# Kernel optimization log

Measured on AMD Instinct MI355X. Metric: run time of the kernel, lower is better.

Reference implementation:

```python
import jax, jax.numpy as jnp
import numpy as np
from jax import lax

FH, FW, STRIDE = 100, 160, 16
IMG_H, IMG_W = FH * STRIDE, FW * STRIDE
A = 9
PRE_NMS, POST_NMS = 6000, 300  # prediction-path caps (training=0)
IOU_THR = 0.7
NEG = jnp.float32(-1e9)


def _make_anchor_map():
    # classic 3 scales x 3 aspect ratios, stride-16 grid, (y1,x1,y2,x2)
    scales = np.array([128.0, 256.0, 512.0], np.float32)
    ratios = np.array([0.5, 1.0, 2.0], np.float32)
    hs = (scales[:, None] * np.sqrt(ratios)[None, :]).reshape(-1)  # [9]
    ws = (scales[:, None] / np.sqrt(ratios)[None, :]).reshape(-1)
    cy = ((np.arange(FH, dtype=np.float32) + 0.5) * STRIDE)[:, None, None]
    cx = ((np.arange(FW, dtype=np.float32) + 0.5) * STRIDE)[None, :, None]
    y1 = np.broadcast_to(cy - 0.5 * hs, (FH, FW, A))
    x1 = np.broadcast_to(cx - 0.5 * ws, (FH, FW, A))
    y2 = np.broadcast_to(cy + 0.5 * hs, (FH, FW, A))
    x2 = np.broadcast_to(cx + 0.5 * ws, (FH, FW, A))
    am = np.stack([y1, x1, y2, x2], axis=-1)  # [FH,FW,9,4]
    return jnp.asarray(am.reshape(1, FH, FW, A * 4))


def setup_inputs() -> dict:
    key = jax.random.key(0)
    ks = jax.random.split(key, 6)
    return {
        "input_image": jax.random.uniform(ks[0], (1, IMG_H, IMG_W, 3), jnp.float32),
        "feature_map": jax.random.normal(ks[1], (1, FH, FW, 512), jnp.float32),
        "anchor_map": _make_anchor_map(),
        "anchor_valid_map": jnp.ones((1, FH, FW, A), jnp.float32),
        "W1": 0.01 * jax.random.normal(ks[2], (3, 3, 512, 512), jnp.float32),
        "b1": jnp.zeros((512,), jnp.float32),
        "Wc": 0.01 * jax.random.normal(ks[3], (1, 1, 512, A), jnp.float32),
        "bc": jnp.zeros((A,), jnp.float32),
        "Wr": 0.01 * jax.random.normal(ks[4], (1, 1, 512, 4 * A), jnp.float32),
        "br": jnp.zeros((4 * A,), jnp.float32),
        "training": 0,
    }


def _conv(x, w, b):
    return lax.conv_general_dilated(
        x, w, (1, 1), "SAME", dimension_numbers=("NHWC", "HWIO", "NHWC")
    ) + b


def _iou_one_vs_all(box, boxes):
    yy1 = jnp.maximum(box[0], boxes[:, 0])
    xx1 = jnp.maximum(box[1], boxes[:, 1])
    yy2 = jnp.minimum(box[2], boxes[:, 2])
    xx2 = jnp.minimum(box[3], boxes[:, 3])
    inter = jnp.maximum(yy2 - yy1, 0.0) * jnp.maximum(xx2 - xx1, 0.0)
    a1 = jnp.maximum(box[2] - box[0], 0.0) * jnp.maximum(box[3] - box[1], 0.0)
    a2 = jnp.maximum(boxes[:, 2] - boxes[:, 0], 0.0) * jnp.maximum(boxes[:, 3] - boxes[:, 1], 0.0)
    return inter / (a1 + a2 - inter + 1e-8)


def _nms(boxes, scores, max_out, iou_thr):
    # greedy NMS with fixed iteration count (padded with zero boxes)
    def step(s, _):
        i = jnp.argmax(s)
        best = s[i]
        box = boxes[i]
        valid = best > NEG * 0.5
        ious = _iou_one_vs_all(box, boxes)
        s = jnp.where(ious > iou_thr, NEG, s)
        s = s.at[i].set(NEG)
        out = jnp.where(valid, box, jnp.zeros_like(box))
        return s, out

    _, sel = lax.scan(step, scores, None, length=max_out)
    return sel  # [max_out, 4]


def reference(input_image, feature_map, anchor_map, anchor_valid_map,
              W1, b1, Wc, bc, Wr, br, training):
    pre_nms = 12000 if training else PRE_NMS
    post_nms = 2000 if training else POST_NMS
    # RPN head convs
    y = jax.nn.relu(_conv(feature_map, W1, b1))
    scores_map = jax.nn.sigmoid(_conv(y, Wc, bc))          # [1,FH,FW,9]
    reg_map = _conv(y, Wr, br)                              # [1,FH,FW,36]
    # flatten (extract_valid)
    anchors = anchor_map.reshape(-1, 4)                     # [N,4] (y1,x1,y2,x2)
    obj = scores_map.reshape(-1)                            # [N]
    deltas = reg_map.reshape(-1, 4)                         # [N,4] (ty,tx,th,tw)
    # delta -> bbox decode (means=0, stds=1)
    ah = anchors[:, 2] - anchors[:, 0]
    aw = anchors[:, 3] - anchors[:, 1]
    acy = anchors[:, 0] + 0.5 * ah
    acx = anchors[:, 1] + 0.5 * aw
    cy = acy + deltas[:, 0] * ah
    cx = acx + deltas[:, 1] * aw
    h = ah * jnp.exp(deltas[:, 2])
    w = aw * jnp.exp(deltas[:, 3])
    props = jnp.stack([cy - 0.5 * h, cx - 0.5 * w, cy + 0.5 * h, cx + 0.5 * w], axis=1)
    # sort desc by score, keep top pre_nms
    sc, idx = lax.top_k(obj, pre_nms)
    props = props[idx]
    # clip to image
    img_h = jnp.float32(input_image.shape[1])
    img_w = jnp.float32(input_image.shape[2])
    tl = jnp.maximum(props[:, 0:2], 0.0)
    y2 = jnp.minimum(props[:, 2], img_h)[:, None]
    x2 = jnp.minimum(props[:, 3], img_w)[:, None]
    props = jnp.concatenate([tl, y2, x2], axis=1)
    # min-size filter (>=16 on each side), via score masking (jit-safe)
    hh = props[:, 2] - props[:, 0]
    ww = props[:, 3] - props[:, 1]
    sc = jnp.where((hh >= 16.0) & (ww >= 16.0), sc, NEG)
    proposals = _nms(props, sc, post_nms, IOU_THR)          # [post_nms,4], zero-padded
    return scores_map, reg_map, proposals
```

## Files before the change

### kernel.cpp

```cpp
#include <hip/hip_runtime.h>
#include <math.h>

#define FHh 100
#define FWw 160
#define CIN 512
#define COUT 512
#define NPIX 16000
#define NANCH 144000
#define PRE_NMS 6000
#define POST_NMS 300
#define EQCAP 8192

typedef double d4 __attribute__((ext_vector_type(4)));

__device__ __forceinline__ unsigned fkey(float x){
  unsigned b = __float_as_uint(x);
  return (b & 0x80000000u) ? ~b : (b | 0x80000000u);
}
__device__ __forceinline__ unsigned long long dkey(double x){
  unsigned long long u = (unsigned long long)__double_as_longlong(x);
  return (u & 0x8000000000000000ull) ? ~u : (u | 0x8000000000000000ull);
}
__device__ __forceinline__ unsigned long long shfl_u64(unsigned long long x, int lane){
  unsigned lo = (unsigned)x, hi = (unsigned)(x >> 32);
  lo = __shfl(lo, lane, 64);
  hi = __shfl(hi, lane, 64);
  return ((unsigned long long)hi << 32) | lo;
}
__device__ __forceinline__ void gload_lds16(const void* g, void* l){
  __builtin_amdgcn_global_load_lds(
      (const __attribute__((address_space(1))) void*)g,
      (__attribute__((address_space(3))) void*)l, 16, 0, 0);
}

__global__ __launch_bounds__(256) void prep_all(
    const float* __restrict__ Wc, const float* __restrict__ Wr, const float* __restrict__ W1,
    double* __restrict__ WcT, double* __restrict__ WrT, double* __restrict__ W64)
{
  const int bid = blockIdx.x;
  if (bid < 90){
    const int gid = bid*256 + threadIdx.x;
    const int n = gid >> 9, ci = gid & 511;
    if (n < 9) WcT[(size_t)n*512 + ci] = (double)Wc[ci*9 + n];
    else       WrT[(size_t)(n-9)*512 + ci] = (double)Wr[ci*36 + (n-9)];
  } else {
    const int i = (bid - 90)*256 + threadIdx.x;
    const float4 v = ((const float4*)W1)[i];
    double2* d = (double2*)(W64 + (size_t)i*4);
    d[0] = make_double2((double)v.x, (double)v.y);
    d[1] = make_double2((double)v.z, (double)v.w);
  }
}

__global__ __launch_bounds__(256, 2) void conv_gemm(
    const float* __restrict__ fm, const double* __restrict__ W64,
    const float* __restrict__ b1, double* __restrict__ yd)
{
  __shared__ double Ns[16*204];
  __shared__ double Bsh[2][16*128];

  const int bid  = blockIdx.x;
  const int cg   = bid / 125;
  const int tile = bid - cg*125;
  const int rp   = tile / 5;
  const int xseg = tile - rp*5;
  const int x0   = xseg*32;
  const int row0 = rp*4;
  const int co0  = cg*128;

  const int tid  = threadIdx.x;
  const int lane = tid & 63;
  const int kl   = lane >> 4;
  const int cl   = lane & 15;
  const int wv   = tid >> 6;
  const int wr   = wv >> 1;
  const int wc   = wv & 1;

  double pf[4][4];

  auto APF_LOAD = [&](int kc){
    #pragma unroll
    for (int it = 0; it < 4; ++it){
      const int t  = it*256 + tid;
      const int px = t >> 2, kq = t & 3;
      const int nr = px / 34, nc = px - nr*34;
      const int row = row0 + nr - 1, col = x0 + nc - 1;
      const bool ok = (t < 816) && (row >= 0) && (row < FHh) && (col >= 0) && (col < FWw);
      if (ok){
        const float4 v = *(const float4*)(fm + ((size_t)(row*FWw + col))*CIN + kc*16 + kq*4);
        pf[it][0] = (double)v.x; pf[it][1] = (double)v.y;
        pf[it][2] = (double)v.z; pf[it][3] = (double)v.w;
      } else {
        pf[it][0] = pf[it][1] = pf[it][2] = pf[it][3] = 0.0;
      }
    }
  };
  auto APF_WRITE = [&](){
    #pragma unroll
    for (int it = 0; it < 4; ++it){
      const int t  = it*256 + tid;
      const int px = t >> 2, kq = t & 3;
      if (t < 816){
        #pragma unroll
        for (int u = 0; u < 4; ++u)
          Ns[(kq*4 + u)*204 + px] = pf[it][u];
      }
    }
  };
  auto BGLDS = [&](int buf, int tap, int kc){
    #pragma unroll
    for (int s = 0; s < 4; ++s){
      const int g    = s*256 + tid;
      const int krow = g >> 6;
      const int co2  = (g & 63)*2;
      const double* src = W64 + ((size_t)(tap*512 + kc*16 + krow))*512 + co0 + co2;
      gload_lds16(src, &Bsh[buf][krow*128 + co2]);
    }
  };

  d4 acc[4][4];
  #pragma unroll
  for (int mt = 0; mt < 4; ++mt)
    #pragma unroll
    for (int nt = 0; nt < 4; ++nt) acc[mt][nt] = (d4){0.0, 0.0, 0.0, 0.0};

  APF_LOAD(0);
  BGLDS(0, 0, 0);
  APF_WRITE();
  __syncthreads();

  const int abase_t = kl*204 + cl;
  const int bbase_t = kl*128 + wc*64 + cl;

  for (int kc = 0; kc < 32; ++kc){
    #pragma unroll 1
    for (int tap = 0; tap < 9; ++tap){
      const int ph  = kc*9 + tap;
      const int cur = ph & 1;
      if (ph + 1 < 288){
        const int ntap = (tap == 8) ? 0 : tap + 1;
        const int nkc  = (tap == 8) ? kc + 1 : kc;
        BGLDS(cur ^ 1, ntap, nkc);
      }
      if (tap == 7 && kc < 31) APF_LOAD(kc + 1);
      const int ty = tap / 3;
      const int dy = ty - 1, dx = (tap - ty*3) - 1;
      const double* An = Ns + abase_t + (wr*2 + dy + 1)*34 + (dx + 1);
      const double* Bn = Bsh[cur] + bbase_t;
      #pragma unroll
      for (int k4 = 0; k4 < 4; ++k4){
        const double a0 = An[k4*4*204 + 0*34 + 0];
        const double a1 = An[k4*4*204 + 0*34 + 16];
        const double a2 = An[k4*4*204 + 1*34 + 0];
        const double a3 = An[k4*4*204 + 1*34 + 16];
        const double b0 = Bn[k4*4*128 + 0];
        const double b1v= Bn[k4*4*128 + 16];
        const double b2 = Bn[k4*4*128 + 32];
        const double b3 = Bn[k4*4*128 + 48];
        acc[0][0] = __builtin_amdgcn_mfma_f64_16x16x4f64(a0, b0,  acc[0][0], 0, 0, 0);
        acc[0][1] = __builtin_amdgcn_mfma_f64_16x16x4f64(a0, b1v, acc[0][1], 0, 0, 0);
        acc[0][2] = __builtin_amdgcn_mfma_f64_16x16x4f64(a0, b2,  acc[0][2], 0, 0, 0);
        acc[0][3] = __builtin_amdgcn_mfma_f64_16x16x4f64(a0, b3,  acc[0][3], 0, 0, 0);
        acc[1][0] = __builtin_amdgcn_mfma_f64_16x16x4f64(a1, b0,  acc[1][0], 0, 0, 0);
        acc[1][1] = __builtin_amdgcn_mfma_f64_16x16x4f64(a1, b1v, acc[1][1], 0, 0, 0);
        acc[1][2] = __builtin_amdgcn_mfma_f64_16x16x4f64(a1, b2,  acc[1][2], 0, 0, 0);
        acc[1][3] = __builtin_amdgcn_mfma_f64_16x16x4f64(a1, b3,  acc[1][3], 0, 0, 0);
        acc[2][0] = __builtin_amdgcn_mfma_f64_16x16x4f64(a2, b0,  acc[2][0], 0, 0, 0);
        acc[2][1] = __builtin_amdgcn_mfma_f64_16x16x4f64(a2, b1v, acc[2][1], 0, 0, 0);
        acc[2][2] = __builtin_amdgcn_mfma_f64_16x16x4f64(a2, b2,  acc[2][2], 0, 0, 0);
        acc[2][3] = __builtin_amdgcn_mfma_f64_16x16x4f64(a2, b3,  acc[2][3], 0, 0, 0);
        acc[3][0] = __builtin_amdgcn_mfma_f64_16x16x4f64(a3, b0,  acc[3][0], 0, 0, 0);
        acc[3][1] = __builtin_amdgcn_mfma_f64_16x16x4f64(a3, b1v, acc[3][1], 0, 0, 0);
        acc[3][2] = __builtin_amdgcn_mfma_f64_16x16x4f64(a3, b2,  acc[3][2], 0, 0, 0);
        acc[3][3] = __builtin_amdgcn_mfma_f64_16x16x4f64(a3, b3,  acc[3][3], 0, 0, 0);
      }
      __syncthreads();
      if (tap == 8 && kc < 31){
        APF_WRITE();
        __syncthreads();
      }
    }
  }
  double bb[4];
  #pragma unroll
  for (int nt = 0; nt < 4; ++nt) bb[nt] = (double)b1[co0 + wc*64 + nt*16 + cl];
  #pragma unroll
  for (int mt = 0; mt < 4; ++mt){
    #pragma unroll
    for (int i = 0; i < 4; ++i){
      const int pxl = wr*64 + mt*16 + 4*i + kl;
      const int gpx = (row0 + (pxl >> 5))*FWw + x0 + (pxl & 31);
      double* yrow = yd + (size_t)gpx*CIN + co0 + wc*64 + cl;
      #pragma unroll
      for (int nt = 0; nt < 4; ++nt){
        yrow[nt*16] = fmax(acc[mt][nt][i] + bb[nt], 0.0);
      }
    }
  }
}

__global__ __launch_bounds__(256) void head2(
    const double* __restrict__ yd, const double* __restrict__ WcT, const float* __restrict__ bc,
    const double* __restrict__ WrT, const float* __restrict__ br,
    float* __restrict__ out, double* __restrict__ scored, double* __restrict__ regd)
{
  __shared__ double yl[8192];
  const int bid = blockIdx.x, t = threadIdx.x;
  const double2* src = (const double2*)(yd + (size_t)bid * 8192);
  double2* dst = (double2*)yl;
  for (int j = t; j < 4096; j += 256) dst[j] = src[j];
  __syncthreads();
  if (t < 180){
    const int n  = t % 45;
    const int pq = t / 45;
    const double* w = (n < 9) ? (WcT + (size_t)n*512) : (WrT + (size_t)(n-9)*512);
    const double* y0 = yl + (pq*4+0)*512;
    const double* y1 = yl + (pq*4+1)*512;
    const double* y2 = yl + (pq*4+2)*512;
    const double* y3 = yl + (pq*4+3)*512;
    double s0=0.0, s1=0.0, s2=0.0, s3=0.0;
    for (int ci = 0; ci < 512; ++ci){
      const double wv = w[ci];
      s0 = fma(y0[ci], wv, s0);
      s1 = fma(y1[ci], wv, s1);
      s2 = fma(y2[ci], wv, s2);
      s3 = fma(y3[ci], wv, s3);
    }
    const double sv[4] = {s0, s1, s2, s3};
    if (n < 9){
      const double bb = (double)bc[n];
      #pragma unroll
      for (int u = 0; u < 4; ++u){
        const double s = sv[u] + bb;
        const double sig = 1.0 / (1.0 + exp(-s));
        const int gi = (bid*16 + pq*4 + u)*9 + n;
        out[gi] = (float)sig;
        scored[gi] = sig;
      }
    } else {
      const int m = n - 9;
      const double bb = (double)br[m];
      #pragma unroll
      for (int u = 0; u < 4; ++u){
        const double s = sv[u] + bb;
        const int gi = (bid*16 + pq*4 + u)*36 + m;
        out[144000 + gi] = (float)s;
        regd[gi] = s;
      }
    }
  }
}

__global__ __launch_bounds__(256) void decode_hist(
    const float* __restrict__ amap, const double* __restrict__ scored,
    const double* __restrict__ regd, double* __restrict__ boxesd,
    unsigned* __restrict__ key32, unsigned long long* __restrict__ nmskey,
    unsigned* __restrict__ hist)
{
  const int i = blockIdx.x*256 + threadIdx.x;
  if (i >= NANCH) return;
  const double a0=(double)amap[4*i+0], a1=(double)amap[4*i+1];
  const double a2=(double)amap[4*i+2], a3=(double)amap[4*i+3];
  const double d0=regd[4*i+0], d1=regd[4*i+1], d2=regd[4*i+2], d3=regd[4*i+3];
  const double ah = a2 - a0, aw = a3 - a1;
  const double cy = a0 + 0.5*ah + d0*ah;
  const double cx = a1 + 0.5*aw + d1*aw;
  const double h = ah * exp(d2), w = aw * exp(d3);
  double y1 = cy - 0.5*h, x1 = cx - 0.5*w, y2 = cy + 0.5*h, x2 = cx + 0.5*w;
  y1 = fmax(y1, 0.0); x1 = fmax(x1, 0.0);
  y2 = fmin(y2, 1600.0); x2 = fmin(x2, 2560.0);
  boxesd[4*i+0]=y1; boxesd[4*i+1]=x1; boxesd[4*i+2]=y2; boxesd[4*i+3]=x2;
  const double obj = scored[i];
  const bool ok = (y2 - y1 >= 16.0) && (x2 - x1 >= 16.0);
  const unsigned k32 = fkey((float)obj);
  key32[i] = k32;
  nmskey[i] = ok ? dkey(obj) : dkey(-1e9);
  atomicAdd(&hist[k32 >> 16], 1u);
}

__global__ __launch_bounds__(1024) void scan_hi(const unsigned* __restrict__ hist, int* __restrict__ meta){
  __shared__ unsigned part[1024];
  const int t = threadIdx.x;
  unsigned s = 0;
  for (int j = 0; j < 64; ++j) s += hist[65535 - (t*64 + j)];
  part[t] = s;
  __syncthreads();
  for (int off = 1; off < 1024; off <<= 1){
    unsigned v = (t >= off) ? part[t - off] : 0u;
    __syncthreads();
    part[t] += v;
    __syncthreads();
  }
  const unsigned incl = part[t], excl = incl - s;
  if (excl < PRE_NMS && incl >= PRE_NMS){
    unsigned cum = excl;
    for (int j = 0; j < 64; ++j){
      const int bin = 65535 - (t*64 + j);
      const unsigned c = hist[bin];
      if (cum + c >= PRE_NMS){ meta[0] = bin; meta[1] = (int)cum; break; }
      cum += c;
    }
  }
}

__global__ __launch_bounds__(256) void hist_lo(const unsigned* __restrict__ key,
                                               const int* __restrict__ meta, unsigned* __restrict__ hist){
  const int i = blockIdx.x*256 + threadIdx.x;
  if (i < NANCH){
    const unsigned k = key[i];
    if ((int)(k >> 16) == meta[0]) atomicAdd(&hist[k & 0xFFFFu], 1u);
  }
}

__global__ __launch_bounds__(1024) void scan_lo(const unsigned* __restrict__ hist, int* __restrict__ meta){
  __shared__ unsigned part[1024];
  const int t = threadIdx.x;
  const unsigned G0 = (unsigned)meta[1];
  unsigned s = 0;
  for (int j = 0; j < 64; ++j) s += hist[65535 - (t*64 + j)];
  part[t] = s;
  __syncthreads();
  for (int off = 1; off < 1024; off <<= 1){
    unsigned v = (t >= off) ? part[t - off] : 0u;
    __syncthreads();
    part[t] += v;
    __syncthreads();
  }
  const unsigned incl = G0 + part[t], excl = incl - s;
  if (excl < PRE_NMS && incl >= PRE_NMS){
    unsigned cum = excl;
    for (int j = 0; j < 64; ++j){
      const int bin = 65535 - (t*64 + j);
      const unsigned c = hist[bin];
      if (cum + c >= PRE_NMS){
        meta[2] = (int)(((unsigned)meta[0] << 16) | (unsigned)bin);
        meta[3] = (int)cum;
        meta[4] = PRE_NMS - (int)cum;
        break;
      }
      cum += c;
    }
  }
}

__global__ __launch_bounds__(256) void compact_k(
    const unsigned* __restrict__ key, const unsigned long long* __restrict__ nmskey,
    const double* __restrict__ boxesd, const int* __restrict__ meta,
    int* __restrict__ cnt, double* __restrict__ selboxd,
    unsigned long long* __restrict__ selkey, int* __restrict__ eqidx)
{
  const int i = blockIdx.x*256 + threadIdx.x;
  if (i >= NANCH) return;
  const unsigned k = key[i];
  const unsigned T = (unsigned)meta[2];
  if (k > T){
    const int s = atomicAdd(&cnt[0], 1);
    selboxd[4*s+0]=boxesd[4*i+0]; selboxd[4*s+1]=boxesd[4*i+1];
    selboxd[4*s+2]=boxesd[4*i+2]; selboxd[4*s+3]=boxesd[4*i+3];
    selkey[s] = nmskey[i];
  } else if (k == T){
    const int e = atomicAdd(&cnt[1], 1);
    if (e < EQCAP) eqidx[e] = i;
  }
}

__global__ __launch_bounds__(256) void rankeq(
    const double* __restrict__ scored, const double* __restrict__ boxesd,
    const unsigned long long* __restrict__ nmskey,
    const int* __restrict__ meta, const int* __restrict__ cnt,
    const int* __restrict__ eqidx, double* __restrict__ selboxd,
    unsigned long long* __restrict__ selkey)
{
  __shared__ int eq[EQCAP];
  const int t = threadIdx.x;
  int E = cnt[1]; if (E > EQCAP) E = EQCAP;
  const int R = meta[4], G2 = meta[3];
  for (int j = t; j < E; j += 256) eq[j] = eqidx[j];
  __syncthreads();
  for (int j = t; j < E; j += 256){
    const int my = eq[j];
    const double smy = scored[my];
    int rank = 0;
    for (int k2 = 0; k2 < E; ++k2){
      const int ok = eq[k2];
      const double sk = scored[ok];
      rank += ((sk > smy) || (sk == smy && ok < my)) ? 1 : 0;
    }
    if (rank < R){
      const int s = G2 + rank;
      selboxd[4*s+0]=boxesd[4*my+0]; selboxd[4*s+1]=boxesd[4*my+1];
      selboxd[4*s+2]=boxesd[4*my+2]; selboxd[4*s+3]=boxesd[4*my+3];
      selkey[s] = nmskey[my];
    }
  }
}

__global__ __launch_bounds__(256) void rank_scatter(
    const unsigned long long* __restrict__ selkey, const double* __restrict__ selboxd,
    unsigned long long* __restrict__ skeys, double* __restrict__ sboxd)
{
  __shared__ unsigned long long k[PRE_NMS];
  const int t = threadIdx.x;
  for (int j = t; j < PRE_NMS; j += 256) k[j] = selkey[j];
  __syncthreads();
  const int j = blockIdx.x*256 + t;
  if (j >= PRE_NMS) return;
  const unsigned long long kj = k[j];
  int r = 0;
  for (int i = 0; i < PRE_NMS; i += 4){
    r += (int)((k[i+0] > kj) || (k[i+0] == kj && (i+0) < j));
    r += (int)((k[i+1] > kj) || (k[i+1] == kj && (i+1) < j));
    r += (int)((k[i+2] > kj) || (k[i+2] == kj && (i+2) < j));
    r += (int)((k[i+3] > kj) || (k[i+3] == kj && (i+3) < j));
  }
  skeys[r] = kj;
  sboxd[(size_t)r*4+0] = selboxd[(size_t)j*4+0];
  sboxd[(size_t)r*4+1] = selboxd[(size_t)j*4+1];
  sboxd[(size_t)r*4+2] = selboxd[(size_t)j*4+2];
  sboxd[(size_t)r*4+3] = selboxd[(size_t)j*4+3];
}

__global__ __launch_bounds__(256) void iou_bitmap(
    const double* __restrict__ sboxd, unsigned long long* __restrict__ rowbits)
{
  __shared__ double cbx[4096];
  const int g = blockIdx.y;
  const int r0 = blockIdx.x * 16;
  const int t = threadIdx.x;
  const int cbase = g * 1024;
  for (int e = t; e < 4096; e += 256){
    const int bi = cbase + (e >> 2);
    cbx[e] = (bi < PRE_NMS) ? sboxd[(size_t)bi*4 + (e & 3)] : 0.0;
  }
  __syncthreads();
  const int r = r0 + (t >> 4);
  const int w = t & 15;
  const double by1 = sboxd[(size_t)r*4+0], bx1 = sboxd[(size_t)r*4+1];
  const double by2 = sboxd[(size_t)r*4+2], bx2 = sboxd[(size_t)r*4+3];
  const double a1 = fmax(by2-by1, 0.0) * fmax(bx2-bx1, 0.0);
  unsigned long long bits = 0ull;
  for (int b = 0; b < 64; ++b){
    const int bcol = (b + w) & 63;
    const int j = cbase + w*64 + bcol;
    if (j < PRE_NMS){
      const int ce = (w*64 + bcol)*4;
      const double c0 = cbx[ce+0], c1 = cbx[ce+1], c2 = cbx[ce+2], c3 = cbx[ce+3];
      const double yy1 = fmax(by1, c0), xx1 = fmax(bx1, c1);
      const double yy2 = fmin(by2, c2), xx2 = fmin(bx2, c3);
      const double inter = fmax(yy2-yy1, 0.0) * fmax(xx2-xx1, 0.0);
      const double a2 = fmax(c2-c0, 0.0) * fmax(c3-c1, 0.0);
      const double iou = inter / (a1 + a2 - inter + 1e-8);
      if (iou > 0.7) bits |= (1ull << bcol);
    }
  }
  rowbits[(size_t)r*128 + g*16 + w] = bits;
}

__global__ __launch_bounds__(64) void greedy(
    const unsigned long long* __restrict__ skeys, const double* __restrict__ sboxd,
    const unsigned long long* __restrict__ rowbits, float* __restrict__ outp)
{
  const int t = threadIdx.x;
  const unsigned long long KEYTH = dkey(-5.0e8);
  int bad = PRE_NMS;
  for (int j = t; j < PRE_NMS; j += 64){
    if (skeys[j] <= KEYTH){ bad = j; break; }
  }
  #pragma unroll
  for (int off = 32; off > 0; off >>= 1){
    const int o = __shfl_down(bad, off, 64);
    bad = (o < bad) ? o : bad;
  }
  const int ilim = __builtin_amdgcn_readfirstlane(bad);

  unsigned long long s0 = 0ull, s1 = 0ull;
  int emitted = 0;
  for (int i = 0; i < ilim && emitted < POST_NMS; ++i){
    const int w = i >> 6, b = i & 63;
    const unsigned long long w0 = shfl_u64(s0, w & 63);
    const unsigned long long w1 = shfl_u64(s1, (w - 64) & 63);
    const unsigned long long word = (w < 64) ? w0 : w1;
    if (!((word >> b) & 1ull)){
      if (t < 4) outp[4*emitted + t] = (float)sboxd[(size_t)i*4 + t];
      s0 |= rowbits[(size_t)i*128 + t];
      if (t < 30) s1 |= rowbits[(size_t)i*128 + 64 + t];
      ++emitted;
    }
  }
  for (int r = emitted; r < POST_NMS; ++r)
    if (t < 4) outp[4*r + t] = 0.f;
}

extern "C" void kernel_launch(void* const* d_in, const int* in_sizes, int n_in,
                              void* d_out, int out_size, void* d_ws, size_t ws_size,
                              hipStream_t stream)
{
  const float* fm   = (const float*)d_in[1];
  const float* amap = (const float*)d_in[2];
  const float* W1   = (const float*)d_in[4];
  const float* b1   = (const float*)d_in[5];
  const float* Wc   = (const float*)d_in[6];
  const float* bc   = (const float*)d_in[7];
  const float* Wr   = (const float*)d_in[8];
  const float* br   = (const float*)d_in[9];
  float* out = (float*)d_out;

  char* base = (char*)d_ws;
  size_t off = 0;
  auto A = [&](size_t n) -> char* {
    char* p = base + off;
    off = (off + n + 255) & ~(size_t)255;
    return p;
  };
  double* yd      = (double*)A(65536000);
  double* W64     = (double*)A(18874368);
  double* WcT     = (double*)A(36864);
  double* WrT     = (double*)A(147456);
  double* scored  = (double*)A(1152000);
  double* regd    = (double*)A(4608000);
  unsigned* histc = (unsigned*)A(524328);
  double* boxesd              = (double*)A(4608000);
  unsigned long long* nmskey  = (unsigned long long*)A(1152000);
  unsigned* key32             = (unsigned*)A(576000);
  double* selboxd             = (double*)A(192000);
  unsigned long long* selkey  = (unsigned long long*)A(48000);
  unsigned long long* skeys   = (unsigned long long*)A(48000);
  double* sboxd               = (double*)A(192000);
  unsigned long long* rowbits = (unsigned long long*)A(6144000);
  int* eqidx                  = (int*)A(32768);

  unsigned* hist1 = histc;
  unsigned* hist2 = histc + 65536;
  int* cnt        = (int*)(histc + 131072);
  int* meta       = cnt + 2;

  hipMemsetAsync(histc, 0, (size_t)524328, stream);

  hipLaunchKernelGGL(prep_all, dim3(2394), dim3(256), 0, stream,
                     Wc, Wr, W1, WcT, WrT, W64);
  hipLaunchKernelGGL(conv_gemm, dim3(500), dim3(256), 0, stream, fm, W64, b1, yd);
  hipLaunchKernelGGL(head2, dim3(1000), dim3(256), 0, stream, yd, WcT, bc, WrT, br, out, scored, regd);
  hipLaunchKernelGGL(decode_hist, dim3((NANCH + 255)/256), dim3(256), 0, stream,
                     amap, scored, regd, boxesd, key32, nmskey, hist1);
  hipLaunchKernelGGL(scan_hi, dim3(1), dim3(1024), 0, stream, hist1, meta);
  hipLaunchKernelGGL(hist_lo, dim3((NANCH + 255)/256), dim3(256), 0, stream, key32, meta, hist2);
  hipLaunchKernelGGL(scan_lo, dim3(1), dim3(1024), 0, stream, hist2, meta);
  hipLaunchKernelGGL(compact_k, dim3((NANCH + 255)/256), dim3(256), 0, stream,
                     key32, nmskey, boxesd, meta, cnt, selboxd, selkey, eqidx);
  hipLaunchKernelGGL(rankeq, dim3(1), dim3(256), 0, stream,
                     scored, boxesd, nmskey, meta, cnt, eqidx, selboxd, selkey);
  hipLaunchKernelGGL(rank_scatter, dim3((PRE_NMS + 255)/256), dim3(256), 0, stream,
                     selkey, selboxd, skeys, sboxd);
  hipLaunchKernelGGL(iou_bitmap, dim3(375, 6), dim3(256), 0, stream, sboxd, rowbits);
  hipLaunchKernelGGL(greedy, dim3(1), dim3(64), 0, stream, skeys, sboxd, rowbits, out + 720000);
}
```

Measured before the change: 2.059 ms.

## Triple-buffer weight tiles with explicit vmcnt waits in conv GEMM

Grows the B (weight) LDS buffer from two stages to three so global-to-LDS loads run two phases ahead. The full __syncthreads after each tap is replaced by partial s_waitcnt vmcnt counts plus raw barriers, so a wave only waits for the tile it is about to use. MFMA sections are also wrapped in s_setprio to raise wave priority during compute. The aim is to hide weight load latency. In exchange it adds LDS use, which may lower occupancy, and the correctness of the hand-tuned vmcnt counts depends on how many loads are in flight.

```diff
diff --git a/kernel.cpp b/kernel.cpp
--- a/kernel.cpp
+++ b/kernel.cpp
@@ -57,7 +57,7 @@
     const float* __restrict__ b1, double* __restrict__ yd)
 {
   __shared__ double Ns[16*204];
-  __shared__ double Bsh[2][16*128];
+  __shared__ double Bsh[3][16*128];
 
   const int bid  = blockIdx.x;
   const int cg   = bid / 125;
@@ -126,27 +126,34 @@
 
   APF_LOAD(0);
   BGLDS(0, 0, 0);
+  BGLDS(1, 1, 0);
   APF_WRITE();
-  __syncthreads();
+  asm volatile("s_waitcnt vmcnt(4) lgkmcnt(0)" ::: "memory");
+  __builtin_amdgcn_s_barrier();
 
   const int abase_t = kl*204 + cl;
   const int bbase_t = kl*128 + wc*64 + cl;
+
+  int ntap = 2, nkc = 0;
+  int bufn = 2;
+  int bufr = 0;
 
   for (int kc = 0; kc < 32; ++kc){
     #pragma unroll 1
     for (int tap = 0; tap < 9; ++tap){
-      const int ph  = kc*9 + tap;
-      const int cur = ph & 1;
-      if (ph + 1 < 288){
-        const int ntap = (tap == 8) ? 0 : tap + 1;
-        const int nkc  = (tap == 8) ? kc + 1 : kc;
-        BGLDS(cur ^ 1, ntap, nkc);
+      const int ph = kc*9 + tap;
+      if (ph + 2 < 288){
+        BGLDS(bufn, ntap, nkc);
+        if (++ntap == 9){ ntap = 0; ++nkc; }
+        if (++bufn == 3) bufn = 0;
       }
       if (tap == 7 && kc < 31) APF_LOAD(kc + 1);
       const int ty = tap / 3;
       const int dy = ty - 1, dx = (tap - ty*3) - 1;
       const double* An = Ns + abase_t + (wr*2 + dy + 1)*34 + (dx + 1);
-      const double* Bn = Bsh[cur] + bbase_t;
+      const double* Bn = Bsh[bufr] + bbase_t;
+      if (++bufr == 3) bufr = 0;
+      __builtin_amdgcn_s_setprio(1);
       #pragma unroll
       for (int k4 = 0; k4 < 4; ++k4){
         const double a0 = An[k4*4*204 + 0*34 + 0];
@@ -174,10 +181,22 @@
         acc[3][2] = __builtin_amdgcn_mfma_f64_16x16x4f64(a3, b2,  acc[3][2], 0, 0, 0);
         acc[3][3] = __builtin_amdgcn_mfma_f64_16x16x4f64(a3, b3,  acc[3][3], 0, 0, 0);
       }
-      __syncthreads();
+      __builtin_amdgcn_s_setprio(0);
       if (tap == 8 && kc < 31){
+        asm volatile("s_waitcnt vmcnt(8)" ::: "memory");
+        __builtin_amdgcn_s_barrier();
         APF_WRITE();
-        __syncthreads();
+        asm volatile("s_waitcnt lgkmcnt(0)" ::: "memory");
+        __builtin_amdgcn_s_barrier();
+      } else if (tap == 7 && kc < 31){
+        asm volatile("s_waitcnt vmcnt(8)" ::: "memory");
+        __builtin_amdgcn_s_barrier();
+      } else if (ph == 286){
+        asm volatile("s_waitcnt vmcnt(0)" ::: "memory");
+        __builtin_amdgcn_s_barrier();
+      } else if (ph < 287){
+        asm volatile("s_waitcnt vmcnt(4)" ::: "memory");
+        __builtin_amdgcn_s_barrier();
       }
     }
   }
```

Result: no change. 2.060 ms (+0.1%).

## Load conv weights directly from fp32 global into registers, drop LDS staging

Applied to the files above, without the earlier changes.

The 3x3 conv GEMM no longer pre-converts W1 to a double copy or stages B tiles through double-buffered LDS with global_load_lds. Each wave now reads its B fragments straight from the fp32 weights into registers, converts them to double, and feeds them to the f64 MFMAs. The per-tap barrier is removed, so there is one sync per k-chunk, and s_setprio raises wave priority around the MFMA block. This removes the 18MB W64 write/read and most barriers, but exposes global load latency on every tap with no explicit prefetch, and puts more reliance on cache hits for weights shared across waves.

```diff
diff --git a/kernel.cpp b/kernel.cpp
--- a/kernel.cpp
+++ b/kernel.cpp
@@ -27,37 +27,22 @@
   hi = __shfl(hi, lane, 64);
   return ((unsigned long long)hi << 32) | lo;
 }
-__device__ __forceinline__ void gload_lds16(const void* g, void* l){
-  __builtin_amdgcn_global_load_lds(
-      (const __attribute__((address_space(1))) void*)g,
-      (__attribute__((address_space(3))) void*)l, 16, 0, 0);
-}
 
 __global__ __launch_bounds__(256) void prep_all(
-    const float* __restrict__ Wc, const float* __restrict__ Wr, const float* __restrict__ W1,
-    double* __restrict__ WcT, double* __restrict__ WrT, double* __restrict__ W64)
-{
-  const int bid = blockIdx.x;
-  if (bid < 90){
-    const int gid = bid*256 + threadIdx.x;
-    const int n = gid >> 9, ci = gid & 511;
-    if (n < 9) WcT[(size_t)n*512 + ci] = (double)Wc[ci*9 + n];
-    else       WrT[(size_t)(n-9)*512 + ci] = (double)Wr[ci*36 + (n-9)];
-  } else {
-    const int i = (bid - 90)*256 + threadIdx.x;
-    const float4 v = ((const float4*)W1)[i];
-    double2* d = (double2*)(W64 + (size_t)i*4);
-    d[0] = make_double2((double)v.x, (double)v.y);
-    d[1] = make_double2((double)v.z, (double)v.w);
-  }
+    const float* __restrict__ Wc, const float* __restrict__ Wr,
+    double* __restrict__ WcT, double* __restrict__ WrT)
+{
+  const int gid = blockIdx.x*256 + threadIdx.x;
+  const int n = gid >> 9, ci = gid & 511;
+  if (n < 9) WcT[(size_t)n*512 + ci] = (double)Wc[ci*9 + n];
+  else       WrT[(size_t)(n-9)*512 + ci] = (double)Wr[ci*36 + (n-9)];
 }
 
 __global__ __launch_bounds__(256, 2) void conv_gemm(
-    const float* __restrict__ fm, const double* __restrict__ W64,
+    const float* __restrict__ fm, const float* __restrict__ W1,
     const float* __restrict__ b1, double* __restrict__ yd)
 {
   __shared__ double Ns[16*204];
-  __shared__ double Bsh[2][16*128];
 
   const int bid  = blockIdx.x;
   const int cg   = bid / 125;
@@ -107,16 +92,6 @@
       }
     }
   };
-  auto BGLDS = [&](int buf, int tap, int kc){
-    #pragma unroll
-    for (int s = 0; s < 4; ++s){
-      const int g    = s*256 + tid;
-      const int krow = g >> 6;
-      const int co2  = (g & 63)*2;
-      const double* src = W64 + ((size_t)(tap*512 + kc*16 + krow))*512 + co0 + co2;
-      gload_lds16(src, &Bsh[buf][krow*128 + co2]);
-    }
-  };
 
   d4 acc[4][4];
   #pragma unroll
@@ -125,38 +100,38 @@
     for (int nt = 0; nt < 4; ++nt) acc[mt][nt] = (d4){0.0, 0.0, 0.0, 0.0};
 
   APF_LOAD(0);
-  BGLDS(0, 0, 0);
   APF_WRITE();
   __syncthreads();
 
   const int abase_t = kl*204 + cl;
-  const int bbase_t = kl*128 + wc*64 + cl;
-
+  const float* Bbase = W1 + (size_t)kl*512 + co0 + wc*64 + cl;
+
+  #pragma unroll 1
   for (int kc = 0; kc < 32; ++kc){
     #pragma unroll 1
     for (int tap = 0; tap < 9; ++tap){
-      const int ph  = kc*9 + tap;
-      const int cur = ph & 1;
-      if (ph + 1 < 288){
-        const int ntap = (tap == 8) ? 0 : tap + 1;
-        const int nkc  = (tap == 8) ? kc + 1 : kc;
-        BGLDS(cur ^ 1, ntap, nkc);
-      }
       if (tap == 7 && kc < 31) APF_LOAD(kc + 1);
+      const float* Bt = Bbase + ((size_t)(tap*512 + kc*16))*512;
+      double breg[16];
+      #pragma unroll
+      for (int k4 = 0; k4 < 4; ++k4)
+        #pragma unroll
+        for (int nt = 0; nt < 4; ++nt)
+          breg[k4*4 + nt] = (double)Bt[k4*2048 + nt*16];
       const int ty = tap / 3;
       const int dy = ty - 1, dx = (tap - ty*3) - 1;
       const double* An = Ns + abase_t + (wr*2 + dy + 1)*34 + (dx + 1);
-      const double* Bn = Bsh[cur] + bbase_t;
+      __builtin_amdgcn_s_setprio(1);
       #pragma unroll
       for (int k4 = 0; k4 < 4; ++k4){
         const double a0 = An[k4*4*204 + 0*34 + 0];
         const double a1 = An[k4*4*204 + 0*34 + 16];
         const double a2 = An[k4*4*204 + 1*34 + 0];
         const double a3 = An[k4*4*204 + 1*34 + 16];
-        const double b0 = Bn[k4*4*128 + 0];
-        const double b1v= Bn[k4*4*128 + 16];
-        const double b2 = Bn[k4*4*128 + 32];
-        const double b3 = Bn[k4*4*128 + 48];
+        const double b0 = breg[k4*4 + 0];
+        const double b1v= breg[k4*4 + 1];
+        const double b2 = breg[k4*4 + 2];
+        const double b3 = breg[k4*4 + 3];
         acc[0][0] = __builtin_amdgcn_mfma_f64_16x16x4f64(a0, b0,  acc[0][0], 0, 0, 0);
         acc[0][1] = __builtin_amdgcn_mfma_f64_16x16x4f64(a0, b1v, acc[0][1], 0, 0, 0);
         acc[0][2] = __builtin_amdgcn_mfma_f64_16x16x4f64(a0, b2,  acc[0][2], 0, 0, 0);
@@ -174,11 +149,12 @@
         acc[3][2] = __builtin_amdgcn_mfma_f64_16x16x4f64(a3, b2,  acc[3][2], 0, 0, 0);
         acc[3][3] = __builtin_amdgcn_mfma_f64_16x16x4f64(a3, b3,  acc[3][3], 0, 0, 0);
       }
+      __builtin_amdgcn_s_setprio(0);
+    }
+    __syncthreads();
+    if (kc < 31){
+      APF_WRITE();
       __syncthreads();
-      if (tap == 8 && kc < 31){
-        APF_WRITE();
-        __syncthreads();
-      }
     }
   }
   double bb[4];
@@ -513,7 +489,6 @@
     return p;
   };
   double* yd      = (double*)A(65536000);
-  double* W64     = (double*)A(18874368);
   double* WcT     = (double*)A(36864);
   double* WrT     = (double*)A(147456);
   double* scored  = (double*)A(1152000);
@@ -536,9 +511,9 @@
 
   hipMemsetAsync(histc, 0, (size_t)524328, stream);
 
-  hipLaunchKernelGGL(prep_all, dim3(2394), dim3(256), 0, stream,
-                     Wc, Wr, W1, WcT, WrT, W64);
-  hipLaunchKernelGGL(conv_gemm, dim3(500), dim3(256), 0, stream, fm, W64, b1, yd);
+  hipLaunchKernelGGL(prep_all, dim3(90), dim3(256), 0, stream,
+                     Wc, Wr, WcT, WrT);
+  hipLaunchKernelGGL(conv_gemm, dim3(500), dim3(256), 0, stream, fm, W1, b1, yd);
   hipLaunchKernelGGL(head2, dim3(1000), dim3(256), 0, stream, yd, WcT, bc, WrT, br, out, scored, regd);
   hipLaunchKernelGGL(decode_hist, dim3((NANCH + 255)/256), dim3(256), 0, stream,
                      amap, scored, regd, boxesd, key32, nmskey, hist1);
```

Result: no change. 2.020 ms (-1.9%).
